# Optimization experiments

Measured on AMD Instinct MI355X. Metric: run time of the kernel, lower is better.

## Reference

```python
import jax, jax.numpy as jnp
import numpy as np


def conv1d(x, w, b, pad):
    # x: [B, Cin, T], w: [Cout, Cin, K]
    y = jax.lax.conv_general_dilated(x, w, window_strides=(1,), padding=[(pad, pad)],
                                     dimension_numbers=('NCH', 'OIH', 'NCH'))
    return y + b[None, :, None]


def setup_inputs() -> dict:
    key = jax.random.key(0)
    ks = jax.random.split(key, 16)
    B, T1, T2 = 32, 2048, 512
    Cmel, Ctext, Catt = 100, 512, 100
    s = 0.05
    inp = {
        'queries': jax.random.normal(ks[0], (B, Cmel, T1), dtype=jnp.float32),
        'keys': jax.random.normal(ks[1], (B, Ctext, T2), dtype=jnp.float32),
        'query_lens': jax.random.randint(ks[2], (B,), 1, T1),
        'mask': jax.random.randint(ks[3], (B, T2, 1), 0, 2).astype(bool),
        'attn_prior': jax.random.uniform(ks[4], (B, T1, T2), dtype=jnp.float32),
        # key_proj: ConvNorm(512->1024, k=3) -> ReLU -> ConvNorm(1024->100, k=1)
        'kW1': jax.random.normal(ks[5], (Ctext * 2, Ctext, 3), dtype=jnp.float32) * s,
        'kb1': jnp.zeros((Ctext * 2,), dtype=jnp.float32),
        'kW2': jax.random.normal(ks[6], (Catt, Ctext * 2, 1), dtype=jnp.float32) * s,
        'kb2': jnp.zeros((Catt,), dtype=jnp.float32),
        # query_proj: ConvNorm(100->200, k=3) -> ReLU -> ConvNorm(200->100, k=1) -> ReLU -> ConvNorm(100->100, k=1)
        'qW1': jax.random.normal(ks[7], (Cmel * 2, Cmel, 3), dtype=jnp.float32) * s,
        'qb1': jnp.zeros((Cmel * 2,), dtype=jnp.float32),
        'qW2': jax.random.normal(ks[8], (Cmel, Cmel * 2, 1), dtype=jnp.float32) * s,
        'qb2': jnp.zeros((Cmel,), dtype=jnp.float32),
        'qW3': jax.random.normal(ks[9], (Catt, Cmel, 1), dtype=jnp.float32) * s,
        'qb3': jnp.zeros((Catt,), dtype=jnp.float32),
    }
    return inp


def reference(queries, keys, query_lens, mask, attn_prior,
              kW1, kb1, kW2, kb2, qW1, qb1, qW2, qb2, qW3, qb3):
    # key projection -> [B, Catt, T2]
    k = jax.nn.relu(conv1d(keys, kW1, kb1, 1))
    k = conv1d(k, kW2, kb2, 0)
    # query projection -> [B, Catt, T1]
    q = jax.nn.relu(conv1d(queries, qW1, qb1, 1))
    q = jax.nn.relu(conv1d(q, qW2, qb2, 0))
    q = conv1d(q, qW3, qb3, 0)
    q2 = jnp.sum(q * q, axis=1)                      # [B, T1]
    k2 = jnp.sum(k * k, axis=1)                      # [B, T2]
    qk = jnp.einsum('bct,bcs->bts', q, k)            # [B, T1, T2]
    attn = -0.0005 * (q2[:, :, None] + k2[:, None, :] - 2.0 * qk)[:, None]  # [B,1,T1,T2]
    attn = jax.nn.log_softmax(attn, axis=3) + jnp.log(attn_prior[:, None] + 1e-8)
    attn_logprob = attn
    m = jnp.transpose(mask, (0, 2, 1))[:, :, None, :]  # [B,1,1,T2], True = masked
    attn = jnp.where(m, -jnp.inf, attn)
    attn = jax.nn.softmax(attn, axis=3)
    return attn, attn_logprob
```

## Files before the change

### kernel.cpp

```cpp
#include <hip/hip_runtime.h>
#include <cstdint>

#define B_   32
#define T1_  2048
#define T2_  512

typedef __attribute__((ext_vector_type(8))) short short8;
typedef __attribute__((ext_vector_type(4))) float f32x4;

__device__ __forceinline__ unsigned short f2bf(float f) {
    union { float f; unsigned u; } x; x.f = f;
    unsigned r = x.u + 0x7fffu + ((x.u >> 16) & 1u);
    return (unsigned short)(r >> 16);
}
__device__ __forceinline__ float bf2f(unsigned short u) {
    union { unsigned u; float f; } x; x.u = ((unsigned)u) << 16;
    return x.f;
}

__device__ __forceinline__ void async16(const unsigned short* g, unsigned short* l) {
    __builtin_amdgcn_global_load_lds(
        (const __attribute__((address_space(1))) unsigned int*)g,
        (__attribute__((address_space(3))) unsigned int*)l, 16, 0, 0);
}

__global__ __launch_bounds__(256) void prep_kernel(
    const float* __restrict__ queries, const float* __restrict__ keys,
    const float* __restrict__ kW1, const float* __restrict__ kW2,
    const float* __restrict__ qW1, const float* __restrict__ qW2,
    const float* __restrict__ qW3,
    unsigned short* __restrict__ keysT, unsigned short* __restrict__ queriesT,
    unsigned short* __restrict__ Wdst)
{
    __shared__ float tile[32][33];
    const int blk = blockIdx.x, tid = threadIdx.x;
    if (blk < 16384) {
        const float* X; unsigned short* Y; int C, Cp, T, ntx, tx, ty, b;
        if (blk < 8192) {
            X = keys; Y = keysT; C = 512; Cp = 512; T = 512; ntx = 16;
            b = blk >> 8; int rem = blk & 255; ty = rem >> 4; tx = rem & 15;
        } else {
            int f = blk - 8192;
            X = queries; Y = queriesT; C = 100; Cp = 128; T = 2048; ntx = 64;
            b = f >> 8; int rem = f & 255; tx = rem >> 2; ty = rem & 3;
        }
        const int c0 = ty * 32, t0 = tx * 32;
        const int cl = tid >> 5, tl = tid & 31;
#pragma unroll
        for (int i = 0; i < 4; ++i) {
            int c = c0 + cl + i * 8;
            float v = (c < C) ? X[((size_t)b * C + c) * T + t0 + tl] : 0.f;
            tile[cl + i * 8][tl] = v;
        }
        __syncthreads();
#pragma unroll
        for (int i = 0; i < 4; ++i) {
            int tw = cl + i * 8, cw = tl;
            Y[((size_t)b * (T + 2) + t0 + tw + 1) * Cp + c0 + cw] = f2bf(tile[cw][tw]);
        }
        if (tid < 32) {
            if (tx == 0)       Y[((size_t)b * (T + 2)) * Cp + c0 + tid] = 0;
            if (tx == ntx - 1) Y[((size_t)b * (T + 2) + T + 1) * Cp + c0 + tid] = 0;
        }
    } else {
        size_t base = (size_t)(blk - 16384) * 2048 + (size_t)tid * 8;
#pragma unroll
        for (int j = 0; j < 8; ++j) {
            size_t idx = base + j;
            float v = 0.f;
            if (idx < 1572864) {
                int dk = (int)(idx / 524288); int rem = (int)(idx % 524288);
                int m = rem >> 9, ci = rem & 511;
                v = kW1[((size_t)m * 512 + ci) * 3 + dk];
            } else if (idx < 1703936) {
                int r = (int)(idx - 1572864); int m = r >> 10, c = r & 1023;
                if (m < 100) v = kW2[(size_t)m * 1024 + c];
            } else if (idx < 1802240) {
                int r = (int)(idx - 1703936); int dk = r / 32768, rem = r % 32768;
                int m = rem >> 7, ci = rem & 127;
                if (m < 200 && ci < 100) v = qW1[((size_t)m * 100 + ci) * 3 + dk];
            } else if (idx < 1835008) {
                int r = (int)(idx - 1802240); int m = r >> 8, c = r & 255;
                if (m < 100 && c < 200) v = qW2[(size_t)m * 200 + c];
            } else if (idx < 1851392) {
                int r = (int)(idx - 1835008); int m = r >> 7, c = r & 127;
                if (m < 100 && c < 100) v = qW3[(size_t)m * 100 + c];
            } else {
                continue;
            }
            Wdst[idx] = f2bf(v);
        }
    }
}

struct GArgs {
    const unsigned short* A;
    const unsigned short* Bm;
    const float* bias;
    unsigned short* Y;
    float* nrm;
    int Ck, N, Mpad, nx, relu, norm, Cout;
};

template<int KW>
__global__ __launch_bounds__(256) void gemm_pair(GArgs g0, GArgs g1, int n0)
{
    __shared__ __align__(16) unsigned char smem[36352];
    unsigned short* Al = (unsigned short*)smem;
    unsigned short* Bl = Al + 4096;
    unsigned short* Ct = (unsigned short*)smem;
    float* biasS = (float*)(smem + 34816);
    float* normS = (float*)(smem + 35328);

    const bool first = (blockIdx.x < (unsigned)n0);
    const GArgs g = first ? g0 : g1;
    const int idx = first ? blockIdx.x : (blockIdx.x - n0);
    const int ny = g.Mpad >> 7;
    const int per_b = g.nx * ny;
    const int b = idx / per_b; const int rem = idx - b * per_b;
    const int y = rem / g.nx, x = rem - y * g.nx;
    const int co0 = y * 128, t0 = x * 128;

    const int tid = threadIdx.x;
    const int wave = tid >> 6, lane = tid & 63;
    const int lm = lane & 15, kg = lane >> 4;
    const int mbase = (wave >> 1) * 64, nbase = (wave & 1) * 64;

    if (tid < 128) biasS[tid] = (co0 + tid < g.Cout) ? g.bias[co0 + tid] : 0.f;

    const int rL = lane >> 2;
    const int cA = (lane & 3) * 8;
    const int Ck = g.Ck;

    f32x4 acc[4][4];
#pragma unroll
    for (int mi = 0; mi < 4; ++mi)
#pragma unroll
        for (int ni = 0; ni < 4; ++ni) acc[mi][ni] = (f32x4){0.f, 0.f, 0.f, 0.f};

#pragma unroll 1
    for (int dk = 0; dk < KW; ++dk) {
        const unsigned short* Ad = g.A + ((size_t)dk * g.Mpad + co0) * Ck;
        const unsigned short* Bd = g.Bm +
            ((size_t)b * (g.N + (KW == 3 ? 2 : 0)) + t0 + dk) * Ck;
        for (int kk = 0; kk < Ck; kk += 32) {
            __syncthreads();
#pragma unroll
            for (int i = 0; i < 2; ++i) {
                int R0 = i * 64 + wave * 16;
                async16(Ad + (size_t)(R0 + rL) * Ck + kk + cA, Al + R0 * 32);
                async16(Bd + (size_t)(R0 + rL) * Ck + kk + cA, Bl + R0 * 32);
            }
            __syncthreads();
            short8 av[4], bv[4];
#pragma unroll
            for (int mi = 0; mi < 4; ++mi)
                av[mi] = *(const short8*)(Al + (mbase + mi * 16 + lm) * 32 + kg * 8);
#pragma unroll
            for (int ni = 0; ni < 4; ++ni)
                bv[ni] = *(const short8*)(Bl + (nbase + ni * 16 + lm) * 32 + kg * 8);
#pragma unroll
            for (int mi = 0; mi < 4; ++mi)
#pragma unroll
                for (int ni = 0; ni < 4; ++ni)
                    acc[mi][ni] = __builtin_amdgcn_mfma_f32_16x16x32_bf16(
                        av[mi], bv[ni], acc[mi][ni], 0, 0, 0);
        }
    }
    __syncthreads();

    float sq[4] = {0.f, 0.f, 0.f, 0.f};
#pragma unroll
    for (int mi = 0; mi < 4; ++mi)
#pragma unroll
        for (int ni = 0; ni < 4; ++ni)
#pragma unroll
            for (int r = 0; r < 4; ++r) {
                int co_l = mbase + mi * 16 + kg * 4 + r;
                int t_l  = nbase + ni * 16 + lm;
                float v = acc[mi][ni][r] + biasS[co_l];
                if (g.relu) v = fmaxf(v, 0.f);
                Ct[t_l * 136 + co_l] = f2bf(v);
                sq[ni] += v * v;
            }
    if (g.norm) {
#pragma unroll
        for (int ni = 0; ni < 4; ++ni) {
            float s = sq[ni];
            s += __shfl_xor(s, 16, 64);
            s += __shfl_xor(s, 32, 64);
            if (kg == 0) normS[(wave >> 1) * 128 + nbase + ni * 16 + lm] = s;
        }
    }
    __syncthreads();
    unsigned short* Yb = g.Y + ((size_t)b * g.N + t0) * g.Mpad + co0;
    int c0 = (tid & 15) * 8;
#pragma unroll
    for (int p = 0; p < 8; ++p) {
        int r = (tid >> 4) + p * 16;
        *(uint4*)(Yb + (size_t)r * g.Mpad + c0) = *(const uint4*)(Ct + r * 136 + c0);
    }
    if (g.norm && tid < 128)
        g.nrm[(size_t)b * g.N + t0 + tid] = normS[tid] + normS[128 + tid];
}

__global__ __launch_bounds__(256) void attn_mfma(
    const unsigned short* __restrict__ q,
    const unsigned short* __restrict__ k,
    const float* __restrict__ q2,
    const float* __restrict__ k2,
    const unsigned char* __restrict__ mask,
    const float* __restrict__ prior,
    float* __restrict__ out_attn, float* __restrict__ out_logp)
{
    __shared__ float redM[4][32], redS[4][32];
    __shared__ float rowA[32], rowB[32];

    const int b = blockIdx.y, t0 = blockIdx.x * 32;
    const int tid = threadIdx.x, wave = tid >> 6, lane = tid & 63;
    const int lm = lane & 15, quad = lane >> 4;
    const float NEG_INF = -__builtin_huge_valf();

    const unsigned short* qb = q + ((size_t)b * T1_ + t0) * 128;
    short8 af[2][4];
#pragma unroll
    for (int mi = 0; mi < 2; ++mi)
#pragma unroll
        for (int kb = 0; kb < 4; ++kb)
            af[mi][kb] = *(const short8*)(qb + (size_t)(mi * 16 + lm) * 128 + kb * 32 + quad * 8);

    f32x4 acc[2][8];
#pragma unroll
    for (int mi = 0; mi < 2; ++mi)
#pragma unroll
        for (int nf = 0; nf < 8; ++nf) acc[mi][nf] = (f32x4){0.f, 0.f, 0.f, 0.f};

    const unsigned short* kp = k + ((size_t)b * T2_ + wave * 128) * 128;
#pragma unroll
    for (int nf = 0; nf < 8; ++nf) {
        short8 bfr[4];
#pragma unroll
        for (int kb = 0; kb < 4; ++kb)
            bfr[kb] = *(const short8*)(kp + (size_t)(nf * 16 + lm) * 128 + kb * 32 + quad * 8);
#pragma unroll
        for (int mi = 0; mi < 2; ++mi)
#pragma unroll
            for (int kb = 0; kb < 4; ++kb)
                acc[mi][nf] = __builtin_amdgcn_mfma_f32_16x16x32_bf16(
                    af[mi][kb], bfr[kb], acc[mi][nf], 0, 0, 0);
    }

    float k2v[8];
    unsigned char mk[8];
#pragma unroll
    for (int nf = 0; nf < 8; ++nf) {
        int col = wave * 128 + nf * 16 + lm;
        k2v[nf] = k2[b * T2_ + col];
        mk[nf]  = mask[b * T2_ + col];
    }
    float q2v[2][4];
#pragma unroll
    for (int mi = 0; mi < 2; ++mi)
#pragma unroll
        for (int r = 0; r < 4; ++r)
            q2v[mi][r] = q2[b * T1_ + t0 + mi * 16 + quad * 4 + r];
#pragma unroll
    for (int mi = 0; mi < 2; ++mi)
#pragma unroll
        for (int nf = 0; nf < 8; ++nf)
#pragma unroll
            for (int r = 0; r < 4; ++r)
                acc[mi][nf][r] = 1e-3f * acc[mi][nf][r] - 5e-4f * (q2v[mi][r] + k2v[nf]);

#pragma unroll
    for (int mi = 0; mi < 2; ++mi)
#pragma unroll
        for (int r = 0; r < 4; ++r) {
            float m = NEG_INF;
#pragma unroll
            for (int nf = 0; nf < 8; ++nf) m = fmaxf(m, acc[mi][nf][r]);
#pragma unroll
            for (int d = 1; d <= 8; d <<= 1) m = fmaxf(m, __shfl_xor(m, d, 64));
            float s = 0.f;
#pragma unroll
            for (int nf = 0; nf < 8; ++nf) s += __expf(acc[mi][nf][r] - m);
#pragma unroll
            for (int d = 1; d <= 8; d <<= 1) s += __shfl_xor(s, d, 64);
            if (lm == 0) {
                redM[wave][mi * 16 + quad * 4 + r] = m;
                redS[wave][mi * 16 + quad * 4 + r] = s;
            }
        }
    __syncthreads();
    if (tid < 32) {
        float m = redM[0][tid];
        m = fmaxf(m, redM[1][tid]); m = fmaxf(m, redM[2][tid]); m = fmaxf(m, redM[3][tid]);
        float s = 0.f;
#pragma unroll
        for (int w = 0; w < 4; ++w) s += redS[w][tid] * __expf(redM[w][tid] - m);
        rowA[tid] = m + __logf(s);
    }
    __syncthreads();
    float L1[2][4];
#pragma unroll
    for (int mi = 0; mi < 2; ++mi)
#pragma unroll
        for (int r = 0; r < 4; ++r) L1[mi][r] = rowA[mi * 16 + quad * 4 + r];

    const size_t base = ((size_t)b * T1_ + t0) * T2_;
#pragma unroll
    for (int mi = 0; mi < 2; ++mi)
#pragma unroll
        for (int r = 0; r < 4; ++r) {
            size_t rowoff = base + (size_t)(mi * 16 + quad * 4 + r) * T2_;
#pragma unroll
            for (int nf = 0; nf < 8; ++nf) {
                int col = wave * 128 + nf * 16 + lm;
                float pv = prior[rowoff + col];
                float t = acc[mi][nf][r] + __logf(pv + 1e-8f);
                out_logp[rowoff + col] = t - L1[mi][r];
                acc[mi][nf][r] = mk[nf] ? NEG_INF : t;
            }
        }

#pragma unroll
    for (int mi = 0; mi < 2; ++mi)
#pragma unroll
        for (int r = 0; r < 4; ++r) {
            float m = NEG_INF;
#pragma unroll
            for (int nf = 0; nf < 8; ++nf) m = fmaxf(m, acc[mi][nf][r]);
#pragma unroll
            for (int d = 1; d <= 8; d <<= 1) m = fmaxf(m, __shfl_xor(m, d, 64));
            float s = 0.f;
#pragma unroll
            for (int nf = 0; nf < 8; ++nf) s += __expf(acc[mi][nf][r] - m);
#pragma unroll
            for (int d = 1; d <= 8; d <<= 1) s += __shfl_xor(s, d, 64);
            if (lm == 0) {
                redM[wave][mi * 16 + quad * 4 + r] = m;
                redS[wave][mi * 16 + quad * 4 + r] = s;
            }
        }
    __syncthreads();
    if (tid < 32) {
        float m = redM[0][tid];
        m = fmaxf(m, redM[1][tid]); m = fmaxf(m, redM[2][tid]); m = fmaxf(m, redM[3][tid]);
        float s = 0.f;
#pragma unroll
        for (int w = 0; w < 4; ++w) s += redS[w][tid] * __expf(redM[w][tid] - m);
        rowA[tid] = m;
        rowB[tid] = 1.0f / s;
    }
    __syncthreads();

#pragma unroll
    for (int mi = 0; mi < 2; ++mi)
#pragma unroll
        for (int r = 0; r < 4; ++r) {
            int rl = mi * 16 + quad * 4 + r;
            float m2 = rowA[rl], is2 = rowB[rl];
            size_t rowoff = base + (size_t)rl * T2_;
#pragma unroll
            for (int nf = 0; nf < 8; ++nf) {
                int col = wave * 128 + nf * 16 + lm;
                out_attn[rowoff + col] = __expf(acc[mi][nf][r] - m2) * is2;
            }
        }
}

extern "C" void kernel_launch(void* const* d_in, const int* in_sizes, int n_in,
                              void* d_out, int out_size, void* d_ws, size_t ws_size,
                              hipStream_t stream)
{
    const float* queries = (const float*)d_in[0];
    const float* keys    = (const float*)d_in[1];
    const unsigned char* mask = (const unsigned char*)d_in[3];
    const float* prior   = (const float*)d_in[4];
    const float* kW1 = (const float*)d_in[5];
    const float* kb1 = (const float*)d_in[6];
    const float* kW2 = (const float*)d_in[7];
    const float* kb2 = (const float*)d_in[8];
    const float* qW1 = (const float*)d_in[9];
    const float* qb1 = (const float*)d_in[10];
    const float* qW2 = (const float*)d_in[11];
    const float* qb2 = (const float*)d_in[12];
    const float* qW3 = (const float*)d_in[13];
    const float* qb3 = (const float*)d_in[14];

    unsigned short* ws = (unsigned short*)d_ws;
    unsigned short* keysT    = ws;
    unsigned short* queriesT = ws + 8421376;
    unsigned short* Bmat2    = ws + 16818176;
    unsigned short* Bmat4    = ws + 33595392;
    unsigned short* Bmat5    = ws + 50372608;
    unsigned short* q_att    = ws + 58761216;
    unsigned short* k_att    = ws + 67149824;
    unsigned short* Wdst     = ws + 69246976;
    unsigned short* Wk1s = Wdst;
    unsigned short* Wk2  = Wdst + 1572864;
    unsigned short* Wq1s = Wdst + 1703936;
    unsigned short* Wq2  = Wdst + 1802240;
    unsigned short* Wq3  = Wdst + 1835008;
    float* q2f = (float*)(ws + 71098368);
    float* k2f = q2f + 65536;

    float* out_attn = (float*)d_out;
    float* out_logp = (float*)d_out + (size_t)B_ * T1_ * T2_;

    dim3 blk(256);
    prep_kernel<<<dim3(17408), blk, 0, stream>>>(queries, keys, kW1, kW2, qW1, qW2, qW3,
                                                 keysT, queriesT, Wdst);

    GArgs a_key1 = {Wk1s, keysT,    kb1, Bmat2, nullptr, 512,  512, 1024,  4, 1, 0, 1024};
    GArgs a_q1   = {Wq1s, queriesT, qb1, Bmat4, nullptr, 128, 2048,  256, 16, 1, 0,  200};
    gemm_pair<3><<<dim3(2048), blk, 0, stream>>>(a_key1, a_q1, 1024);

    GArgs a_key2 = {Wk2, Bmat2, kb2, k_att, k2f,     1024,  512, 128,  4, 0, 1, 100};
    GArgs a_q2   = {Wq2, Bmat4, qb2, Bmat5, nullptr,  256, 2048, 128, 16, 1, 0, 100};
    gemm_pair<1><<<dim3(640), blk, 0, stream>>>(a_key2, a_q2, 128);

    GArgs a_q3   = {Wq3, Bmat5, qb3, q_att, q2f, 128, 2048, 128, 16, 0, 1, 100};
    gemm_pair<1><<<dim3(512), blk, 0, stream>>>(a_q3, a_q3, 512);

    attn_mfma<<<dim3(T1_ / 32, B_), blk, 0, stream>>>(q_att, k_att, q2f, k2f, mask, prior,
                                                      out_attn, out_logp);

    (void)in_sizes; (void)n_in; (void)out_size; (void)ws_size;
}
```

Measured before the change: 616.0 us.

## Double GEMM K-step with XOR-swizzled LDS and coarsen prep transpose blocks

The projection GEMMs now load 64-wide K slices per barrier pair instead of 32. The LDS rows are XOR-swizzled to avoid bank conflicts on the short8 fragment reads. This halves the number of syncthreads per K loop, at the cost of twice the LDS footprint for the A/B staging. Separately, each prep-kernel transpose block now handles four time tiles in a loop, cutting the grid from 17408 to 5120 blocks.

```diff
diff --git a/kernel.cpp b/kernel.cpp
--- a/kernel.cpp
+++ b/kernel.cpp
@@ -34,36 +34,40 @@
 {
     __shared__ float tile[32][33];
     const int blk = blockIdx.x, tid = threadIdx.x;
-    if (blk < 16384) {
-        const float* X; unsigned short* Y; int C, Cp, T, ntx, tx, ty, b;
-        if (blk < 8192) {
+    if (blk < 4096) {
+        const float* X; unsigned short* Y; int C, Cp, T, ntx, ty, tx0, b;
+        if (blk < 2048) {
             X = keys; Y = keysT; C = 512; Cp = 512; T = 512; ntx = 16;
-            b = blk >> 8; int rem = blk & 255; ty = rem >> 4; tx = rem & 15;
+            b = blk >> 6; int rem = blk & 63; ty = rem >> 2; tx0 = (rem & 3) * 4;
         } else {
-            int f = blk - 8192;
+            int f = blk - 2048;
             X = queries; Y = queriesT; C = 100; Cp = 128; T = 2048; ntx = 64;
-            b = f >> 8; int rem = f & 255; tx = rem >> 2; ty = rem & 3;
-        }
-        const int c0 = ty * 32, t0 = tx * 32;
+            b = f >> 6; int rem = f & 63; ty = rem & 3; tx0 = (rem >> 2) * 4;
+        }
+        const int c0 = ty * 32;
         const int cl = tid >> 5, tl = tid & 31;
-#pragma unroll
-        for (int i = 0; i < 4; ++i) {
-            int c = c0 + cl + i * 8;
-            float v = (c < C) ? X[((size_t)b * C + c) * T + t0 + tl] : 0.f;
-            tile[cl + i * 8][tl] = v;
-        }
-        __syncthreads();
-#pragma unroll
-        for (int i = 0; i < 4; ++i) {
-            int tw = cl + i * 8, cw = tl;
-            Y[((size_t)b * (T + 2) + t0 + tw + 1) * Cp + c0 + cw] = f2bf(tile[cw][tw]);
-        }
-        if (tid < 32) {
-            if (tx == 0)       Y[((size_t)b * (T + 2)) * Cp + c0 + tid] = 0;
-            if (tx == ntx - 1) Y[((size_t)b * (T + 2) + T + 1) * Cp + c0 + tid] = 0;
+        for (int tx = tx0; tx < tx0 + 4; ++tx) {
+            const int t0 = tx * 32;
+            __syncthreads();
+#pragma unroll
+            for (int i = 0; i < 4; ++i) {
+                int c = c0 + cl + i * 8;
+                float v = (c < C) ? X[((size_t)b * C + c) * T + t0 + tl] : 0.f;
+                tile[cl + i * 8][tl] = v;
+            }
+            __syncthreads();
+#pragma unroll
+            for (int i = 0; i < 4; ++i) {
+                int tw = cl + i * 8, cw = tl;
+                Y[((size_t)b * (T + 2) + t0 + tw + 1) * Cp + c0 + cw] = f2bf(tile[cw][tw]);
+            }
+            if (tid < 32) {
+                if (tx == 0)       Y[((size_t)b * (T + 2)) * Cp + c0 + tid] = 0;
+                if (tx == ntx - 1) Y[((size_t)b * (T + 2) + T + 1) * Cp + c0 + tid] = 0;
+            }
         }
     } else {
-        size_t base = (size_t)(blk - 16384) * 2048 + (size_t)tid * 8;
+        size_t base = (size_t)(blk - 4096) * 2048 + (size_t)tid * 8;
 #pragma unroll
         for (int j = 0; j < 8; ++j) {
             size_t idx = base + j;
@@ -107,7 +111,7 @@
 {
     __shared__ __align__(16) unsigned char smem[36352];
     unsigned short* Al = (unsigned short*)smem;
-    unsigned short* Bl = Al + 4096;
+    unsigned short* Bl = Al + 8192;
     unsigned short* Ct = (unsigned short*)smem;
     float* biasS = (float*)(smem + 34816);
     float* normS = (float*)(smem + 35328);
@@ -128,8 +132,9 @@
 
     if (tid < 128) biasS[tid] = (co0 + tid < g.Cout) ? g.bias[co0 + tid] : 0.f;
 
-    const int rL = lane >> 2;
-    const int cA = (lane & 3) * 8;
+    const int r7 = lane >> 3;
+    const int s7 = lane & 7;
+    const int swz = ((s7 ^ r7) * 8);
     const int Ck = g.Ck;
 
     f32x4 acc[4][4];
@@ -143,28 +148,37 @@
         const unsigned short* Ad = g.A + ((size_t)dk * g.Mpad + co0) * Ck;
         const unsigned short* Bd = g.Bm +
             ((size_t)b * (g.N + (KW == 3 ? 2 : 0)) + t0 + dk) * Ck;
-        for (int kk = 0; kk < Ck; kk += 32) {
+        for (int kk = 0; kk < Ck; kk += 64) {
             __syncthreads();
 #pragma unroll
-            for (int i = 0; i < 2; ++i) {
-                int R0 = i * 64 + wave * 16;
-                async16(Ad + (size_t)(R0 + rL) * Ck + kk + cA, Al + R0 * 32);
-                async16(Bd + (size_t)(R0 + rL) * Ck + kk + cA, Bl + R0 * 32);
+            for (int i = 0; i < 4; ++i) {
+                int R0 = wave * 32 + i * 8;
+                async16(Ad + (size_t)(R0 + r7) * Ck + kk + swz, Al + R0 * 64);
+                async16(Bd + (size_t)(R0 + r7) * Ck + kk + swz, Bl + R0 * 64);
             }
             __syncthreads();
-            short8 av[4], bv[4];
-#pragma unroll
-            for (int mi = 0; mi < 4; ++mi)
-                av[mi] = *(const short8*)(Al + (mbase + mi * 16 + lm) * 32 + kg * 8);
-#pragma unroll
-            for (int ni = 0; ni < 4; ++ni)
-                bv[ni] = *(const short8*)(Bl + (nbase + ni * 16 + lm) * 32 + kg * 8);
-#pragma unroll
-            for (int mi = 0; mi < 4; ++mi)
-#pragma unroll
-                for (int ni = 0; ni < 4; ++ni)
-                    acc[mi][ni] = __builtin_amdgcn_mfma_f32_16x16x32_bf16(
-                        av[mi], bv[ni], acc[mi][ni], 0, 0, 0);
+#pragma unroll
+            for (int kk2 = 0; kk2 < 2; ++kk2) {
+                short8 av[4], bv[4];
+#pragma unroll
+                for (int mi = 0; mi < 4; ++mi) {
+                    int row = mbase + mi * 16 + lm;
+                    av[mi] = *(const short8*)(Al + row * 64 +
+                                              (((kk2 * 4 + kg) ^ (lm & 7)) * 8));
+                }
+#pragma unroll
+                for (int ni = 0; ni < 4; ++ni) {
+                    int row = nbase + ni * 16 + lm;
+                    bv[ni] = *(const short8*)(Bl + row * 64 +
+                                              (((kk2 * 4 + kg) ^ (lm & 7)) * 8));
+                }
+#pragma unroll
+                for (int mi = 0; mi < 4; ++mi)
+#pragma unroll
+                    for (int ni = 0; ni < 4; ++ni)
+                        acc[mi][ni] = __builtin_amdgcn_mfma_f32_16x16x32_bf16(
+                            av[mi], bv[ni], acc[mi][ni], 0, 0, 0);
+            }
         }
     }
     __syncthreads();
@@ -409,8 +423,8 @@
     float* out_logp = (float*)d_out + (size_t)B_ * T1_ * T2_;
 
     dim3 blk(256);
-    prep_kernel<<<dim3(17408), blk, 0, stream>>>(queries, keys, kW1, kW2, qW1, qW2, qW3,
-                                                 keysT, queriesT, Wdst);
+    prep_kernel<<<dim3(5120), blk, 0, stream>>>(queries, keys, kW1, kW2, qW1, qW2, qW3,
+                                                keysT, queriesT, Wdst);
 
     GArgs a_key1 = {Wk1s, keysT,    kb1, Bmat2, nullptr, 512,  512, 1024,  4, 1, 0, 1024};
     GArgs a_q1   = {Wq1s, queriesT, qb1, Bmat4, nullptr, 128, 2048,  256, 16, 1, 0,  200};
```

After: 597.0 us. 3.1% less time.
